# Kernel tuning notes

Hardware: AMD Instinct MI355X
Metric: run time of the kernel (lower is better)

Reference implementation:

```python
import jax, jax.numpy as jnp
import numpy as np

B_, S, D_IN, D_OUT, N_ADP, R = 4, 4096, 2048, 2048, 4, 16
SCALE = 32.0 / 16.0  # lora_alpha / r, use_rslora=False, same for all adaptors


def setup_inputs() -> dict:
    key = jax.random.key(0)
    ks = jax.random.split(key, 6)
    x = jax.random.normal(ks[0], (B_, S, D_IN), dtype=jnp.float32)
    mask = jax.random.uniform(ks[1], (N_ADP, B_, S, 1), dtype=jnp.float32)
    W = jax.random.normal(ks[2], (D_OUT, D_IN), dtype=jnp.float32) * 0.02
    b = jnp.zeros((D_OUT,), dtype=jnp.float32)
    A = jax.random.normal(ks[3], (N_ADP, R, D_IN), dtype=jnp.float32) * 0.02
    Bw = jax.random.normal(ks[4], (N_ADP, D_OUT, R), dtype=jnp.float32) * 0.02
    return {"x": x, "mask": mask, "W": W, "b": b, "A": A, "Bw": Bw}


def reference(x, mask, W, b, A, Bw):
    # base_layer: y = x @ W^T + b  -> [B, S, D_OUT]
    result = jnp.einsum('bsd,od->bso', x, W) + b
    # all adaptors batched: h = lora_A(x) -> [N, B, S, R]
    h = jnp.einsum('bsd,nrd->nbsr', x, A)
    # delta = lora_B(h) -> [N, B, S, D_OUT]
    delta = jnp.einsum('nbsr,nor->nbso', h, Bw)
    # scale, per-adaptor mask multiply, accumulate into residual
    result = result + jnp.sum(delta * SCALE * mask, axis=0)
    return result
```

## Files before the change

kernel.cpp:

```cpp
#include <hip/hip_runtime.h>
#include <stdint.h>


typedef __attribute__((ext_vector_type(8))) short bf16x8;
typedef __attribute__((ext_vector_type(4))) float f32x4;
typedef __attribute__((ext_vector_type(4))) unsigned short u16x4;
typedef __attribute__((ext_vector_type(8))) unsigned short u16x8;

#define GAS __attribute__((address_space(1)))
#define LAS __attribute__((address_space(3)))

static constexpr int BB   = 4;
static constexpr int SS   = 4096;
static constexpr int DIN  = 2048;
static constexpr int DOUT = 2048;
static constexpr int NADP = 4;
static constexpr int RR   = 16;
static constexpr int M    = BB * SS;
static constexpr int KA   = DIN + NADP * RR;
static constexpr float SCALE = 2.0f;

static_assert(KA % 64 == 0, "K-loop needs BK=64 divisibility");

__device__ __forceinline__ unsigned short f2bf(float f) {
  union { float f; uint32_t u; } v; v.f = f;
  uint32_t u = v.u;
  return (unsigned short)((u + 0x7FFFu + ((u >> 16) & 1u)) >> 16);
}

__global__ __launch_bounds__(256) void pass1_xcvt_h(
    const float* __restrict__ x, const float* __restrict__ A,
    const float* __restrict__ mask, unsigned short* __restrict__ Xaug)
{
  __shared__ unsigned short xb[64 * 64];
  __shared__ unsigned short ab[64 * 64];

  const int tid = threadIdx.x;
  const int rowBase = blockIdx.x * 64;
  const int w = tid >> 6, lane = tid & 63;
  const int quad = lane >> 4, m16 = lane & 15;

  f32x4 acc[4];
  #pragma unroll
  for (int j = 0; j < 4; ++j) acc[j] = f32x4{0.f, 0.f, 0.f, 0.f};

  for (int kc = 0; kc < DIN; kc += 64) {
    __syncthreads();
    #pragma unroll
    for (int l = 0; l < 4; ++l) {
      int v = l * 256 + tid;
      int r = v >> 4;
      int k = (v & 15) * 4;
      float4 xv = *(const float4*)(x + (size_t)(rowBase + r) * DIN + kc + k);
      u16x4 xq = { f2bf(xv.x), f2bf(xv.y), f2bf(xv.z), f2bf(xv.w) };
      *(u16x4*)(xb + r * 64 + k) = xq;
      *(u16x4*)(Xaug + (size_t)(rowBase + r) * KA + kc + k) = xq;
      float4 av = *(const float4*)(A + (size_t)r * DIN + kc + k);
      u16x4 aq = { f2bf(av.x), f2bf(av.y), f2bf(av.z), f2bf(av.w) };
      *(u16x4*)(ab + r * 64 + k) = aq;
    }
    __syncthreads();
    #pragma unroll
    for (int s = 0; s < 2; ++s) {
      bf16x8 af = *(const bf16x8*)(xb + (w * 16 + m16) * 64 + s * 32 + quad * 8);
      #pragma unroll
      for (int jt = 0; jt < 4; ++jt) {
        bf16x8 bfg = *(const bf16x8*)(ab + (jt * 16 + m16) * 64 + s * 32 + quad * 8);
        acc[jt] = __builtin_amdgcn_mfma_f32_16x16x32_bf16(af, bfg, acc[jt], 0, 0, 0);
      }
    }
  }

  const int grow0 = rowBase + w * 16 + quad * 4;
  #pragma unroll
  for (int jt = 0; jt < 4; ++jt) {
    #pragma unroll
    for (int r = 0; r < 4; ++r) {
      int grow = grow0 + r;
      float h = acc[jt][r] * mask[(size_t)jt * M + grow];
      Xaug[(size_t)grow * KA + DIN + jt * 16 + m16] = f2bf(h);
    }
  }
}

__global__ __launch_bounds__(256) void pass2_wcvt(
    const float* __restrict__ W, const float* __restrict__ Bw,
    unsigned short* __restrict__ Waug)
{
  const int idx = blockIdx.x * 256 + threadIdx.x;
  const int row = idx >> 8;
  const int k   = (idx & 255) * 8;
  float4 a = *(const float4*)(W + (size_t)row * DIN + k);
  float4 b = *(const float4*)(W + (size_t)row * DIN + k + 4);
  u16x8 q = { f2bf(a.x), f2bf(a.y), f2bf(a.z), f2bf(a.w),
              f2bf(b.x), f2bf(b.y), f2bf(b.z), f2bf(b.w) };
  *(u16x8*)(Waug + (size_t)row * KA + k) = q;

  if (idx < DOUT * NADP) {
    const int col = idx >> 2, n = idx & 3;
    const float* src = Bw + (size_t)n * DOUT * RR + (size_t)col * RR;
    #pragma unroll
    for (int t = 0; t < 4; ++t) {
      float4 bv = *(const float4*)(src + 4 * t);
      u16x4 qq = { f2bf(SCALE * bv.x), f2bf(SCALE * bv.y),
                   f2bf(SCALE * bv.z), f2bf(SCALE * bv.w) };
      *(u16x4*)(Waug + (size_t)col * KA + DIN + n * 16 + 4 * t) = qq;
    }
  }
}

__global__ __launch_bounds__(256, 3) void gemm_aug(
    const unsigned short* __restrict__ Xa, const unsigned short* __restrict__ Wa,
    const float* __restrict__ bias, float* __restrict__ out)
{
  __shared__ unsigned short lds_a[128 * 64];
  __shared__ unsigned short lds_b[128 * 64];

  const int tid = threadIdx.x;
  const int bn = blockIdx.x, bm = blockIdx.y;
  const int w = tid >> 6, lane = tid & 63;
  const int wm = w >> 1, wn = w & 1;
  const int quad = lane >> 4, m16 = lane & 15;

  f32x4 acc[4][4];
  #pragma unroll
  for (int i = 0; i < 4; ++i)
    #pragma unroll
    for (int j = 0; j < 4; ++j) acc[i][j] = f32x4{0.f, 0.f, 0.f, 0.f};

  const unsigned short* ga = Xa + (size_t)bm * 128 * KA;
  const unsigned short* gb = Wa + (size_t)bn * 128 * KA;

  size_t goff[4];
  int ldso[4];
  #pragma unroll
  for (int l = 0; l < 4; ++l) {
    int p = l * 256 + tid;
    int r = p >> 3;
    int c = (p & 7) ^ (r & 7);
    goff[l] = (size_t)r * KA + c * 8;
    ldso[l] = (l * 256 + (tid & ~63)) * 8;
  }

  for (int k0 = 0; k0 < KA; k0 += 64) {
    __syncthreads();
    #pragma unroll
    for (int l = 0; l < 4; ++l) {
      __builtin_amdgcn_global_load_lds((const GAS void*)(ga + goff[l] + k0),
                                       (LAS void*)(lds_a + ldso[l]), 16, 0, 0);
      __builtin_amdgcn_global_load_lds((const GAS void*)(gb + goff[l] + k0),
                                       (LAS void*)(lds_b + ldso[l]), 16, 0, 0);
    }
    __syncthreads();

    #pragma unroll
    for (int s = 0; s < 2; ++s) {
      const int cc = ((s * 4 + quad) ^ (m16 & 7)) * 8;
      bf16x8 af[4], bfg[4];
      #pragma unroll
      for (int i = 0; i < 4; ++i)
        af[i] = *(const bf16x8*)(lds_a + (wm * 64 + i * 16 + m16) * 64 + cc);
      #pragma unroll
      for (int j = 0; j < 4; ++j)
        bfg[j] = *(const bf16x8*)(lds_b + (wn * 64 + j * 16 + m16) * 64 + cc);
      #pragma unroll
      for (int i = 0; i < 4; ++i)
        #pragma unroll
        for (int j = 0; j < 4; ++j)
          acc[i][j] = __builtin_amdgcn_mfma_f32_16x16x32_bf16(af[i], bfg[j],
                                                              acc[i][j], 0, 0, 0);
    }
  }

  float bv[4];
  #pragma unroll
  for (int j = 0; j < 4; ++j) bv[j] = bias[bn * 128 + wn * 64 + j * 16 + m16];
  #pragma unroll
  for (int i = 0; i < 4; ++i) {
    const int row0 = bm * 128 + wm * 64 + i * 16 + quad * 4;
    #pragma unroll
    for (int j = 0; j < 4; ++j) {
      const int col = bn * 128 + wn * 64 + j * 16 + m16;
      #pragma unroll
      for (int r = 0; r < 4; ++r)
        out[(size_t)(row0 + r) * DOUT + col] = acc[i][j][r] + bv[j];
    }
  }
}

extern "C" void kernel_launch(void* const* d_in, const int* in_sizes, int n_in,
                              void* d_out, int out_size, void* d_ws, size_t ws_size,
                              hipStream_t stream) {
  const float* x    = (const float*)d_in[0];
  const float* mask = (const float*)d_in[1];
  const float* W    = (const float*)d_in[2];
  const float* bias = (const float*)d_in[3];
  const float* A    = (const float*)d_in[4];
  const float* Bw   = (const float*)d_in[5];
  float* out = (float*)d_out;

  unsigned short* Xaug = (unsigned short*)d_ws;
  unsigned short* Waug = Xaug + (size_t)M * KA;

  pass1_xcvt_h<<<dim3(M / 64), dim3(256), 0, stream>>>(x, A, mask, Xaug);
  pass2_wcvt<<<dim3((DOUT * (DIN / 8)) / 256), dim3(256), 0, stream>>>(W, Bw, Waug);
  gemm_aug<<<dim3(DOUT / 128, M / 128), dim3(256), 0, stream>>>(Xaug, Waug, bias, out);
}
```

Measured before the change: 469.6 us.

## Split x conversion from LoRA-A projection and shrink h blocks to 16 rows

The conversion of x and W to bf16 moves into a separate grid-stride kernel, and the Bw scaling is folded into the same kernel. The LoRA-A projection kernel now handles 16 rows per block, with each wave computing one adaptor, so the grid grows from 256 to 1024 blocks. The aim is better occupancy and bandwidth in the pre-pass stages. In exchange, x is read from global memory twice (once for conversion, once for h), and each small block reloads the full A matrix per K chunk, which adds redundant traffic.

```diff
diff --git a/kernel.cpp b/kernel.cpp
--- a/kernel.cpp
+++ b/kernel.cpp
@@ -20,92 +20,97 @@
 static constexpr int KA   = DIN + NADP * RR;
 static constexpr float SCALE = 2.0f;
 
-static_assert(KA % 64 == 0, "K-loop needs BK=64 divisibility");
-
 __device__ __forceinline__ unsigned short f2bf(float f) {
   union { float f; uint32_t u; } v; v.f = f;
   uint32_t u = v.u;
   return (unsigned short)((u + 0x7FFFu + ((u >> 16) & 1u)) >> 16);
 }
 
-__global__ __launch_bounds__(256) void pass1_xcvt_h(
+__device__ __forceinline__ u16x8 cvt8(float4 a, float4 b) {
+  return u16x8{ f2bf(a.x), f2bf(a.y), f2bf(a.z), f2bf(a.w),
+                f2bf(b.x), f2bf(b.y), f2bf(b.z), f2bf(b.w) };
+}
+
+__global__ __launch_bounds__(256) void pass0_convert(
+    const float* __restrict__ x, const float* __restrict__ W,
+    const float* __restrict__ Bw, unsigned short* __restrict__ Xaug,
+    unsigned short* __restrict__ Waug)
+{
+  const int nth = gridDim.x * 256;
+  const int t0 = blockIdx.x * 256 + threadIdx.x;
+
+  const int XCH = M * (DIN / 8);
+  for (int c = t0; c < XCH; c += nth) {
+    int row = c >> 8, k = (c & 255) * 8;
+    float4 a = *(const float4*)(x + (size_t)row * DIN + k);
+    float4 b = *(const float4*)(x + (size_t)row * DIN + k + 4);
+    *(u16x8*)(Xaug + (size_t)row * KA + k) = cvt8(a, b);
+  }
+  const int WCH = DOUT * (DIN / 8);
+  for (int c = t0; c < WCH; c += nth) {
+    int row = c >> 8, k = (c & 255) * 8;
+    float4 a = *(const float4*)(W + (size_t)row * DIN + k);
+    float4 b = *(const float4*)(W + (size_t)row * DIN + k + 4);
+    *(u16x8*)(Waug + (size_t)row * KA + k) = cvt8(a, b);
+  }
+  const int BCH = DOUT * NADP * 2;
+  for (int c = t0; c < BCH; c += nth) {
+    int cn = c >> 1, half = c & 1;
+    int col = cn >> 2, n = cn & 3;
+    const float* src = Bw + ((size_t)n * DOUT + col) * RR + half * 8;
+    float4 a = *(const float4*)src;
+    float4 b = *(const float4*)(src + 4);
+    float4 sa = { SCALE * a.x, SCALE * a.y, SCALE * a.z, SCALE * a.w };
+    float4 sb = { SCALE * b.x, SCALE * b.y, SCALE * b.z, SCALE * b.w };
+    *(u16x8*)(Waug + (size_t)col * KA + DIN + n * 16 + half * 8) = cvt8(sa, sb);
+  }
+}
+
+__global__ __launch_bounds__(256) void pass1_h(
     const float* __restrict__ x, const float* __restrict__ A,
     const float* __restrict__ mask, unsigned short* __restrict__ Xaug)
 {
-  __shared__ unsigned short xb[64 * 64];
+  __shared__ unsigned short xb[16 * 64];
   __shared__ unsigned short ab[64 * 64];
 
   const int tid = threadIdx.x;
-  const int rowBase = blockIdx.x * 64;
+  const int rowBase = blockIdx.x * 16;
   const int w = tid >> 6, lane = tid & 63;
   const int quad = lane >> 4, m16 = lane & 15;
 
-  f32x4 acc[4];
-  #pragma unroll
-  for (int j = 0; j < 4; ++j) acc[j] = f32x4{0.f, 0.f, 0.f, 0.f};
+  f32x4 acc = f32x4{0.f, 0.f, 0.f, 0.f};
 
   for (int kc = 0; kc < DIN; kc += 64) {
     __syncthreads();
+    {
+      int r = tid >> 4, kch = tid & 15;
+      float4 xv = *(const float4*)(x + (size_t)(rowBase + r) * DIN + kc + kch * 4);
+      *(u16x4*)(xb + r * 64 + kch * 4) =
+          u16x4{ f2bf(xv.x), f2bf(xv.y), f2bf(xv.z), f2bf(xv.w) };
+    }
     #pragma unroll
     for (int l = 0; l < 4; ++l) {
       int v = l * 256 + tid;
       int r = v >> 4;
       int k = (v & 15) * 4;
-      float4 xv = *(const float4*)(x + (size_t)(rowBase + r) * DIN + kc + k);
-      u16x4 xq = { f2bf(xv.x), f2bf(xv.y), f2bf(xv.z), f2bf(xv.w) };
-      *(u16x4*)(xb + r * 64 + k) = xq;
-      *(u16x4*)(Xaug + (size_t)(rowBase + r) * KA + kc + k) = xq;
       float4 av = *(const float4*)(A + (size_t)r * DIN + kc + k);
-      u16x4 aq = { f2bf(av.x), f2bf(av.y), f2bf(av.z), f2bf(av.w) };
-      *(u16x4*)(ab + r * 64 + k) = aq;
+      *(u16x4*)(ab + r * 64 + k) =
+          u16x4{ f2bf(av.x), f2bf(av.y), f2bf(av.z), f2bf(av.w) };
     }
     __syncthreads();
     #pragma unroll
     for (int s = 0; s < 2; ++s) {
-      bf16x8 af = *(const bf16x8*)(xb + (w * 16 + m16) * 64 + s * 32 + quad * 8);
-      #pragma unroll
-      for (int jt = 0; jt < 4; ++jt) {
-        bf16x8 bfg = *(const bf16x8*)(ab + (jt * 16 + m16) * 64 + s * 32 + quad * 8);
-        acc[jt] = __builtin_amdgcn_mfma_f32_16x16x32_bf16(af, bfg, acc[jt], 0, 0, 0);
-      }
-    }
-  }
-
-  const int grow0 = rowBase + w * 16 + quad * 4;
-  #pragma unroll
-  for (int jt = 0; jt < 4; ++jt) {
-    #pragma unroll
-    for (int r = 0; r < 4; ++r) {
-      int grow = grow0 + r;
-      float h = acc[jt][r] * mask[(size_t)jt * M + grow];
-      Xaug[(size_t)grow * KA + DIN + jt * 16 + m16] = f2bf(h);
-    }
-  }
-}
-
-__global__ __launch_bounds__(256) void pass2_wcvt(
-    const float* __restrict__ W, const float* __restrict__ Bw,
-    unsigned short* __restrict__ Waug)
-{
-  const int idx = blockIdx.x * 256 + threadIdx.x;
-  const int row = idx >> 8;
-  const int k   = (idx & 255) * 8;
-  float4 a = *(const float4*)(W + (size_t)row * DIN + k);
-  float4 b = *(const float4*)(W + (size_t)row * DIN + k + 4);
-  u16x8 q = { f2bf(a.x), f2bf(a.y), f2bf(a.z), f2bf(a.w),
-              f2bf(b.x), f2bf(b.y), f2bf(b.z), f2bf(b.w) };
-  *(u16x8*)(Waug + (size_t)row * KA + k) = q;
-
-  if (idx < DOUT * NADP) {
-    const int col = idx >> 2, n = idx & 3;
-    const float* src = Bw + (size_t)n * DOUT * RR + (size_t)col * RR;
-    #pragma unroll
-    for (int t = 0; t < 4; ++t) {
-      float4 bv = *(const float4*)(src + 4 * t);
-      u16x4 qq = { f2bf(SCALE * bv.x), f2bf(SCALE * bv.y),
-                   f2bf(SCALE * bv.z), f2bf(SCALE * bv.w) };
-      *(u16x4*)(Waug + (size_t)col * KA + DIN + n * 16 + 4 * t) = qq;
-    }
+      bf16x8 xf = *(const bf16x8*)(xb + m16 * 64 + s * 32 + quad * 8);
+      bf16x8 af = *(const bf16x8*)(ab + (w * 16 + m16) * 64 + s * 32 + quad * 8);
+      acc = __builtin_amdgcn_mfma_f32_16x16x32_bf16(xf, af, acc, 0, 0, 0);
+    }
+  }
+
+  #pragma unroll
+  for (int r = 0; r < 4; ++r) {
+    int grow = rowBase + quad * 4 + r;
+    float h = acc[r] * mask[(size_t)w * M + grow];
+    Xaug[(size_t)grow * KA + DIN + w * 16 + m16] = f2bf(h);
   }
 }
 
@@ -202,7 +207,7 @@
   unsigned short* Xaug = (unsigned short*)d_ws;
   unsigned short* Waug = Xaug + (size_t)M * KA;
 
-  pass1_xcvt_h<<<dim3(M / 64), dim3(256), 0, stream>>>(x, A, mask, Xaug);
-  pass2_wcvt<<<dim3((DOUT * (DIN / 8)) / 256), dim3(256), 0, stream>>>(W, Bw, Waug);
+  pass0_convert<<<dim3(2048), dim3(256), 0, stream>>>(x, W, Bw, Xaug, Waug);
+  pass1_h<<<dim3(M / 16), dim3(256), 0, stream>>>(x, A, mask, Xaug);
   gemm_aug<<<dim3(DOUT / 128, M / 128), dim3(256), 0, stream>>>(Xaug, Waug, bias, out);
 }
```

Measured after the change: 472.7 us. About the same (+0.7%).
